# Performance work log

Hardware: AMD Instinct MI355X
Metric: run time of the kernel (lower is better)

Reference implementation:

```python
import jax, jax.numpy as jnp
import numpy as np

KH = KW = 9
BN_EPS = 1e-5


def conv3x3(x, w):
    # x: [B,Cin,H,W], w: [Cout,Cin,3,3], stride 1, padding 1
    return jax.lax.conv_general_dilated(
        x, w, window_strides=(1, 1), padding=((1, 1), (1, 1)),
        dimension_numbers=("NCHW", "OIHW", "NCHW"))


def cbr(x, w, bn):
    # bn: [4, C] rows = (gamma, beta, running_mean, running_var); inference-mode BN
    g, b, m, v = bn[0], bn[1], bn[2], bn[3]
    x = conv3x3(x, w)
    x = (x - m[:, None, None]) * (g[:, None, None] / jnp.sqrt(v[:, None, None] + BN_EPS)) + b[:, None, None]
    return jax.nn.relu(x)


def weighting(x, atten):
    # x: [B,C,H,W], atten: [B,H,W,KH*KW]
    # out[b,c,h,w] = sum_k atten[b,h,w,k] * x[b,c, h+dh(k), w+dw(k)]  (zero-padded window)
    B, C, H, W = x.shape
    patches = jax.lax.conv_general_dilated_patches(
        x, filter_shape=(KH, KW), window_strides=(1, 1),
        padding=((KH // 2, KH // 2), (KW // 2, KW // 2)))  # [B, C*KH*KW, H, W], channel-major
    patches = patches.reshape(B, C, KH * KW, H, W)
    return jnp.einsum("bckhw,bhwk->bchw", patches, atten)


def _make_params(key, fc_dim=1024):
    d4, d16 = fc_dim // 4, fc_dim // 16
    ks = jax.random.split(key, 16)
    def conv_w(k, co, ci):
        return jax.random.normal(k, (co, ci, 3, 3), jnp.float32) * (1.0 / np.sqrt(ci * 9))
    def bn(k, c):
        g = 1.0 + 0.1 * jax.random.normal(k, (c,), jnp.float32)
        return jnp.stack([g, jnp.zeros((c,)), jnp.zeros((c,)), jnp.ones((c,))])
    p = {}
    p["w1"], p["bn1"] = conv_w(ks[0], d4, fc_dim), bn(ks[1], d4)
    p["w2"], p["bn2"] = conv_w(ks[2], d16, d4), bn(ks[3], d16)
    p["w3"], p["bn3"] = conv_w(ks[4], d4, d16), bn(ks[5], d4)
    p["w4"], p["bn4"] = conv_w(ks[6], d4, fc_dim), bn(ks[7], d4)
    p["w5"], p["bn5"] = conv_w(ks[8], d4, d4), bn(ks[9], d4)
    p["fw1"] = jax.random.normal(ks[10], (10, d4), jnp.float32) * (1.0 / np.sqrt(d4))
    p["fb1"] = jnp.zeros((10,), jnp.float32)
    p["fw2"] = jax.random.normal(ks[11], (1, 10), jnp.float32) * (1.0 / np.sqrt(10))
    p["fb2"] = jnp.zeros((1,), jnp.float32)
    return p


def setup_inputs() -> dict:
    key = jax.random.key(0)
    k1, k2, k3, kp = jax.random.split(key, 4)
    B, fc_dim, H, W = 4, 1024, 64, 64
    inp = {
        "low_key": jax.random.normal(k1, (B, fc_dim, H, W), jnp.float32),
        "low_nonkey": jax.random.normal(k2, (B, fc_dim, H, W), jnp.float32),
        "local_atten": jax.random.uniform(k3, (B, H, W, KH * KW), jnp.float32),
    }
    inp.update(_make_params(kp, fc_dim))
    return inp


def reference(low_key, low_nonkey, local_atten,
              w1, bn1, w2, bn2, w3, bn3, w4, bn4, w5, bn5,
              fw1, fb1, fw2, fb2):
    x = cbr(low_key, w1, bn1)        # [B, 256, H, W]
    x = cbr(x, w2, bn2)              # [B, 64, H, W]
    x = weighting(x, local_atten)    # 9x9 local-attention weighted gather
    x = cbr(x, w3, bn3)              # [B, 256, H, W]
    y = cbr(low_nonkey, w4, bn4)     # [B, 256, H, W]
    out = cbr(x - y, w5, bn5)        # [B, 256, H, W]
    out = out.mean(axis=(2, 3))      # adaptive avg pool to 1x1 -> [B, 256]
    out = out @ fw1.T + fb1          # [B, 10]
    out = out @ fw2.T + fb2          # [B, 1]
    return out
```

## Files before the change

### kernel.cpp

```cpp
#include <hip/hip_runtime.h>
#include <math.h>

typedef _Float16 f16;
typedef f16 f16x8 __attribute__((ext_vector_type(8)));
typedef float f32x4 __attribute__((ext_vector_type(4)));

#define NB 4

__global__ void __launch_bounds__(256)
wtrans_kernel(const float* __restrict__ w, f16* __restrict__ wt, int Co, int Cin) {
  int idx = blockIdx.x * 256 + threadIdx.x;
  int total = Co * Cin * 9;
  if (idx >= total) return;
  int k = idx % 9, t2 = idx / 9;
  int ci = t2 % Cin, co = t2 / Cin;
  wt[((size_t)k * Co + co) * Cin + ci] = (f16)w[idx];
}

__global__ void __launch_bounds__(256)
nchw2nhwc(const float* __restrict__ in, f16* __restrict__ out) {
  __shared__ f16 s[64][66];
  const int t = threadIdx.x;
  const int bh = blockIdx.x, c0 = blockIdx.y * 64;
  const int b = bh >> 6, h = bh & 63;
  const int w = t & 63, cr = t >> 6;
  #pragma unroll
  for (int i = 0; i < 16; ++i) {
    int c = c0 + cr * 16 + i;
    s[cr * 16 + i][w] = (f16)in[(((size_t)b * 1024 + c) * 64 + h) * 64 + w];
  }
  __syncthreads();
  #pragma unroll
  for (int i = 0; i < 2; ++i) {
    int task = t + 256 * i;
    int oct = task & 7, w2 = task >> 3;
    f16x8 v;
    #pragma unroll
    for (int j = 0; j < 8; ++j) v[j] = s[oct * 8 + j][w2];
    *(f16x8*)(out + (((size_t)b * 64 + h) * 64 + w2) * 1024 + c0 + oct * 8) = v;
  }
}

__global__ void __launch_bounds__(256)
conv_mfma(const f16* __restrict__ in, const f16* __restrict__ in2,
          const f16* __restrict__ wt, const float* __restrict__ bn,
          f16* __restrict__ out, float* __restrict__ partial,
          int Cin, int Co) {
  __shared__ __align__(16) f16 xs[4][66][40];
  __shared__ __align__(16) f16 ws[9][64][32];
  __shared__ float s_red[4][64];

  const int t = threadIdx.x;
  const int tile = blockIdx.x;
  const int b = tile >> 5;
  const int h0 = (tile & 31) * 2;
  const int co_blk = blockIdx.y * 64;
  const int wid = t >> 6, lane = t & 63;
  const int row_w = wid >> 1, wcol = (wid & 1) * 32;
  const int l15 = lane & 15, lg = lane >> 4;
  const int koff = lg * 8;

  f32x4 acc[4][2];
  #pragma unroll
  for (int m = 0; m < 4; ++m)
    #pragma unroll
    for (int n = 0; n < 2; ++n)
      #pragma unroll
      for (int r = 0; r < 4; ++r) acc[m][n][r] = 0.f;

  const f16* inb = in + (size_t)b * Cin * 4096;
  const f16* inb2 = in2 ? in2 + (size_t)b * Cin * 4096 : nullptr;

  const int octS = t & 3, wS = (t >> 2) & 63;
  const int NC = Cin >> 5;
  f16x8 ireg[4], wreg[9];

  auto load_stage = [&](int ci0) {
    #pragma unroll
    for (int r = 0; r < 4; ++r) {
      int gh = h0 - 1 + r;
      f16x8 v = {};
      if ((unsigned)gh < 64u) {
        size_t off = ((size_t)gh * 64 + wS) * Cin + ci0 + octS * 8;
        v = *(const f16x8*)(inb + off);
        if (inb2) { f16x8 v2 = *(const f16x8*)(inb2 + off); v = v - v2; }
      }
      ireg[r] = v;
    }
    #pragma unroll
    for (int i = 0; i < 9; ++i) {
      int s = t + 256 * i;
      int oct = s & 3, co = (s >> 2) & 63, k = s >> 8;
      wreg[i] = *(const f16x8*)(wt + ((size_t)k * Co + co_blk + co) * Cin + ci0 + oct * 8);
    }
  };
  auto write_stage = [&]() {
    #pragma unroll
    for (int r = 0; r < 4; ++r)
      *(f16x8*)&xs[r][wS + 1][octS * 8] = ireg[r];
    #pragma unroll
    for (int i = 0; i < 9; ++i) {
      int s = t + 256 * i;
      int oct = s & 3, co = (s >> 2) & 63, k = s >> 8;
      *(f16x8*)&ws[k][co][oct * 8] = wreg[i];
    }
  };

  if (t < 32) {
    int r = t >> 3, side = (t >> 2) & 1, oc = t & 3;
    f16x8 z = {};
    *(f16x8*)&xs[r][side * 65][oc * 8] = z;
  }
  load_stage(0);
  write_stage();
  __syncthreads();

  for (int c = 0; c < NC; ++c) {
    if (c + 1 < NC) load_stage((c + 1) << 5);
    #pragma unroll
    for (int tap = 0; tap < 9; ++tap) {
      const int dh = tap / 3 - 1, dw = tap % 3 - 1;
      f16x8 af[4];
      #pragma unroll
      for (int m = 0; m < 4; ++m)
        af[m] = *(const f16x8*)&ws[tap][m * 16 + l15][koff];
      #pragma unroll
      for (int n = 0; n < 2; ++n) {
        const f16x8 bf = *(const f16x8*)&xs[row_w + dh + 1][wcol + n * 16 + l15 + 1 + dw][koff];
        #pragma unroll
        for (int m = 0; m < 4; ++m)
          acc[m][n] = __builtin_amdgcn_mfma_f32_16x16x32_f16(af[m], bf, acc[m][n], 0, 0, 0);
      }
    }
    __syncthreads();
    if (c + 1 < NC) write_stage();
    __syncthreads();
  }

  if (out) {
    f16* str = (f16*)xs;
    #pragma unroll
    for (int m = 0; m < 4; ++m)
      #pragma unroll
      for (int reg = 0; reg < 4; ++reg) {
        const int cwb = m * 16 + lg * 4 + reg;
        const int co = co_blk + cwb;
        float scale = bn[co] / sqrtf(bn[3 * Co + co] + 1e-5f);
        float shift = bn[Co + co] - bn[2 * Co + co] * scale;
        #pragma unroll
        for (int n = 0; n < 2; ++n) {
          float val = fmaxf(fmaf(acc[m][n][reg], scale, shift), 0.f);
          int px = row_w * 64 + wcol + n * 16 + l15;
          str[px * 72 + cwb] = (f16)val;
        }
      }
    __syncthreads();
    #pragma unroll
    for (int i = 0; i < 4; ++i) {
      int task = t + 256 * i;
      int oct = task & 7;
      int rest = task >> 3;
      int w = rest & 63, row = rest >> 6;
      f16x8 v = *(const f16x8*)&str[(row * 64 + w) * 72 + oct * 8];
      *(f16x8*)(out + (((size_t)(b * 64 + h0 + row) * 64) + w) * Co + co_blk + oct * 8) = v;
    }
  } else {
    #pragma unroll
    for (int m = 0; m < 4; ++m)
      #pragma unroll
      for (int reg = 0; reg < 4; ++reg) {
        const int cwb = m * 16 + lg * 4 + reg;
        const int co = co_blk + cwb;
        float scale = bn[co] / sqrtf(bn[3 * Co + co] + 1e-5f);
        float shift = bn[Co + co] - bn[2 * Co + co] * scale;
        float s = fmaxf(fmaf(acc[m][0][reg], scale, shift), 0.f)
                + fmaxf(fmaf(acc[m][1][reg], scale, shift), 0.f);
        s += __shfl_xor(s, 1, 64);
        s += __shfl_xor(s, 2, 64);
        s += __shfl_xor(s, 4, 64);
        s += __shfl_xor(s, 8, 64);
        if (l15 == 0) s_red[wid][cwb] = s;
      }
    __syncthreads();
    if (t < 64) {
      float v = s_red[0][t] + s_red[1][t] + s_red[2][t] + s_red[3][t];
      partial[((size_t)(b * 256) + co_blk + t) * 32 + (tile & 31)] = v;
    }
  }
}

__global__ void __launch_bounds__(256)
weighting_nhwc(const f16* __restrict__ x, const float* __restrict__ atten,
               f16* __restrict__ out) {
  __shared__ float s_a[64 * 81];
  const int h = blockIdx.x, b = blockIdx.y;
  const int t = threadIdx.x;
  for (int idx = t; idx < 64 * 81; idx += 256)
    s_a[idx] = atten[(size_t)((b * 64 + h) * 64) * 81 + idx];
  __syncthreads();

  const int w = t & 63, cg = t >> 6;
  float acc[16];
  #pragma unroll
  for (int j = 0; j < 16; ++j) acc[j] = 0.f;

  for (int dh = -4; dh <= 4; ++dh) {
    int hh = h + dh;
    if ((unsigned)hh >= 64u) continue;
    #pragma unroll
    for (int dw = -4; dw <= 4; ++dw) {
      int ww = w + dw;
      if ((unsigned)ww >= 64u) continue;
      float a = s_a[w * 81 + (dh + 4) * 9 + (dw + 4)];
      const f16* xp = x + (((size_t)b * 64 + hh) * 64 + ww) * 64 + cg * 16;
      f16x8 v0 = *(const f16x8*)xp;
      f16x8 v1 = *(const f16x8*)(xp + 8);
      #pragma unroll
      for (int j = 0; j < 8; ++j) {
        acc[j]     = fmaf(a, (float)v0[j], acc[j]);
        acc[8 + j] = fmaf(a, (float)v1[j], acc[8 + j]);
      }
    }
  }
  f16x8 o0, o1;
  #pragma unroll
  for (int j = 0; j < 8; ++j) { o0[j] = (f16)acc[j]; o1[j] = (f16)acc[8 + j]; }
  f16* op = out + (((size_t)b * 64 + h) * 64 + w) * 64 + cg * 16;
  *(f16x8*)op = o0;
  *(f16x8*)(op + 8) = o1;
}

__global__ void __launch_bounds__(256)
fc_kernel(const float* __restrict__ partial, const float* __restrict__ fw1,
          const float* __restrict__ fb1, const float* __restrict__ fw2,
          const float* __restrict__ fb2, float* __restrict__ outp) {
  const int t = threadIdx.x;
  const int b = t >> 6, lane = t & 63;
  float pooled[4];
  #pragma unroll
  for (int k = 0; k < 4; ++k) {
    int c = lane + 64 * k;
    float s = 0.f;
    #pragma unroll
    for (int p = 0; p < 32; ++p) s += partial[(size_t)(b * 256 + c) * 32 + p];
    pooled[k] = s * (1.f / 4096.f);
  }
  float o = 0.f;
  for (int i = 0; i < 10; ++i) {
    float d = 0.f;
    #pragma unroll
    for (int k = 0; k < 4; ++k) d += pooled[k] * fw1[i * 256 + lane + 64 * k];
    #pragma unroll
    for (int off = 32; off > 0; off >>= 1) d += __shfl_down(d, off, 64);
    o += (d + fb1[i]) * fw2[i];
  }
  if (lane == 0) outp[b] = o + fb2[0];
}

extern "C" void kernel_launch(void* const* d_in, const int* in_sizes, int n_in,
                              void* d_out, int out_size, void* d_ws, size_t ws_size,
                              hipStream_t stream) {
  const float* low_key    = (const float*)d_in[0];
  const float* low_nonkey = (const float*)d_in[1];
  const float* atten      = (const float*)d_in[2];
  const float* w1 = (const float*)d_in[3];  const float* bn1 = (const float*)d_in[4];
  const float* w2 = (const float*)d_in[5];  const float* bn2 = (const float*)d_in[6];
  const float* w3 = (const float*)d_in[7];  const float* bn3 = (const float*)d_in[8];
  const float* w4 = (const float*)d_in[9];  const float* bn4 = (const float*)d_in[10];
  const float* w5 = (const float*)d_in[11]; const float* bn5 = (const float*)d_in[12];
  const float* fw1 = (const float*)d_in[13]; const float* fb1 = (const float*)d_in[14];
  const float* fw2 = (const float*)d_in[15]; const float* fb2 = (const float*)d_in[16];

  f16* T   = (f16*)d_ws;
  f16* X1  = T + 16777216;
  f16* X2  = X1 + 4194304;
  f16* X3  = X2 + 1048576;
  f16* Y   = X3 + 1048576;
  f16* wt1 = Y + 4194304;
  f16* wt2 = wt1 + 2359296;
  f16* wt3 = wt2 + 147456;
  f16* wt4 = wt3 + 147456;
  f16* wt5 = wt4 + 2359296;
  float* P = (float*)(wt5 + 589824);

  dim3 blk(256);
  wtrans_kernel<<<(256 * 1024 * 9 + 255) / 256, blk, 0, stream>>>(w1, wt1, 256, 1024);
  wtrans_kernel<<<(64 * 256 * 9 + 255) / 256, blk, 0, stream>>>(w2, wt2, 64, 256);
  wtrans_kernel<<<(256 * 64 * 9 + 255) / 256, blk, 0, stream>>>(w3, wt3, 256, 64);
  wtrans_kernel<<<(256 * 1024 * 9 + 255) / 256, blk, 0, stream>>>(w4, wt4, 256, 1024);
  wtrans_kernel<<<(256 * 256 * 9 + 255) / 256, blk, 0, stream>>>(w5, wt5, 256, 256);

  nchw2nhwc<<<dim3(256, 16), blk, 0, stream>>>(low_key, T);
  conv_mfma<<<dim3(128, 4), blk, 0, stream>>>(T, nullptr, wt1, bn1, X1, nullptr, 1024, 256);
  conv_mfma<<<dim3(128, 1), blk, 0, stream>>>(X1, nullptr, wt2, bn2, X2, nullptr, 256, 64);
  weighting_nhwc<<<dim3(64, NB), blk, 0, stream>>>(X2, atten, X3);
  conv_mfma<<<dim3(128, 4), blk, 0, stream>>>(X3, nullptr, wt3, bn3, X1, nullptr, 64, 256);
  nchw2nhwc<<<dim3(256, 16), blk, 0, stream>>>(low_nonkey, T);
  conv_mfma<<<dim3(128, 4), blk, 0, stream>>>(T, nullptr, wt4, bn4, Y, nullptr, 1024, 256);
  conv_mfma<<<dim3(128, 4), blk, 0, stream>>>(X1, Y, wt5, bn5, nullptr, P, 256, 256);
  fc_kernel<<<1, 256, 0, stream>>>(P, fw1, fb1, fw2, fb2, (float*)d_out);
}
```

Baseline: 344.7 us.

## Enlarge conv tile to four rows per block and write output directly

Each conv block now computes four output rows instead of two, with each wave owning a full 64-wide row and 16 accumulators. The weight tile staged in LDS is reused across twice as many pixels, and halo overhead per output drops. The epilogue writes f16x4 straight to global memory instead of staging through shared memory. The weight transpose kernel is also reindexed so its writes are coalesced. In exchange the grid is halved (256 blocks for the big convs, 64 for conv2), which may underfill the 256 CUs, and register pressure rises.

```diff
diff --git a/kernel.cpp b/kernel.cpp
--- a/kernel.cpp
+++ b/kernel.cpp
@@ -2,6 +2,7 @@
 #include <math.h>
 
 typedef _Float16 f16;
+typedef f16 f16x4 __attribute__((ext_vector_type(4)));
 typedef f16 f16x8 __attribute__((ext_vector_type(8)));
 typedef float f32x4 __attribute__((ext_vector_type(4)));
 
@@ -12,9 +13,9 @@
   int idx = blockIdx.x * 256 + threadIdx.x;
   int total = Co * Cin * 9;
   if (idx >= total) return;
-  int k = idx % 9, t2 = idx / 9;
-  int ci = t2 % Cin, co = t2 / Cin;
-  wt[((size_t)k * Co + co) * Cin + ci] = (f16)w[idx];
+  int ci = idx % Cin, t2 = idx / Cin;
+  int co = t2 % Co, k = t2 / Co;
+  wt[idx] = (f16)w[((size_t)co * Cin + ci) * 9 + k];
 }
 
 __global__ void __launch_bounds__(256)
@@ -46,38 +47,37 @@
           const f16* __restrict__ wt, const float* __restrict__ bn,
           f16* __restrict__ out, float* __restrict__ partial,
           int Cin, int Co) {
-  __shared__ __align__(16) f16 xs[4][66][40];
+  __shared__ __align__(16) f16 xs[6][66][40];
   __shared__ __align__(16) f16 ws[9][64][32];
   __shared__ float s_red[4][64];
 
   const int t = threadIdx.x;
   const int tile = blockIdx.x;
-  const int b = tile >> 5;
-  const int h0 = (tile & 31) * 2;
+  const int b = tile >> 4;
+  const int h0 = (tile & 15) * 4;
   const int co_blk = blockIdx.y * 64;
   const int wid = t >> 6, lane = t & 63;
-  const int row_w = wid >> 1, wcol = (wid & 1) * 32;
   const int l15 = lane & 15, lg = lane >> 4;
   const int koff = lg * 8;
 
-  f32x4 acc[4][2];
+  f32x4 acc[4][4];
   #pragma unroll
   for (int m = 0; m < 4; ++m)
     #pragma unroll
-    for (int n = 0; n < 2; ++n)
+    for (int n = 0; n < 4; ++n)
       #pragma unroll
       for (int r = 0; r < 4; ++r) acc[m][n][r] = 0.f;
 
   const f16* inb = in + (size_t)b * Cin * 4096;
   const f16* inb2 = in2 ? in2 + (size_t)b * Cin * 4096 : nullptr;
 
-  const int octS = t & 3, wS = (t >> 2) & 63;
+  const int wS = t >> 2, octS = t & 3;
   const int NC = Cin >> 5;
-  f16x8 ireg[4], wreg[9];
+  f16x8 ireg[6], wreg[9];
 
   auto load_stage = [&](int ci0) {
     #pragma unroll
-    for (int r = 0; r < 4; ++r) {
+    for (int r = 0; r < 6; ++r) {
       int gh = h0 - 1 + r;
       f16x8 v = {};
       if ((unsigned)gh < 64u) {
@@ -96,7 +96,7 @@
   };
   auto write_stage = [&]() {
     #pragma unroll
-    for (int r = 0; r < 4; ++r)
+    for (int r = 0; r < 6; ++r)
       *(f16x8*)&xs[r][wS + 1][octS * 8] = ireg[r];
     #pragma unroll
     for (int i = 0; i < 9; ++i) {
@@ -106,7 +106,7 @@
     }
   };
 
-  if (t < 32) {
+  if (t < 48) {
     int r = t >> 3, side = (t >> 2) & 1, oc = t & 3;
     f16x8 z = {};
     *(f16x8*)&xs[r][side * 65][oc * 8] = z;
@@ -125,8 +125,8 @@
       for (int m = 0; m < 4; ++m)
         af[m] = *(const f16x8*)&ws[tap][m * 16 + l15][koff];
       #pragma unroll
-      for (int n = 0; n < 2; ++n) {
-        const f16x8 bf = *(const f16x8*)&xs[row_w + dh + 1][wcol + n * 16 + l15 + 1 + dw][koff];
+      for (int n = 0; n < 4; ++n) {
+        const f16x8 bf = *(const f16x8*)&xs[wid + dh + 1][n * 16 + l15 + 1 + dw][koff];
         #pragma unroll
         for (int m = 0; m < 4; ++m)
           acc[m][n] = __builtin_amdgcn_mfma_f32_16x16x32_f16(af[m], bf, acc[m][n], 0, 0, 0);
@@ -138,53 +138,47 @@
   }
 
   if (out) {
-    f16* str = (f16*)xs;
+    #pragma unroll
+    for (int m = 0; m < 4; ++m) {
+      float sc[4], sh[4];
+      #pragma unroll
+      for (int reg = 0; reg < 4; ++reg) {
+        int co = co_blk + m * 16 + lg * 4 + reg;
+        sc[reg] = bn[co] / sqrtf(bn[3 * Co + co] + 1e-5f);
+        sh[reg] = bn[Co + co] - bn[2 * Co + co] * sc[reg];
+      }
+      #pragma unroll
+      for (int n = 0; n < 4; ++n) {
+        f16x4 v;
+        #pragma unroll
+        for (int reg = 0; reg < 4; ++reg)
+          v[reg] = (f16)fmaxf(fmaf(acc[m][n][reg], sc[reg], sh[reg]), 0.f);
+        *(f16x4*)(out + ((size_t)(b * 64 + h0 + wid) * 64 + n * 16 + l15) * Co
+                      + co_blk + m * 16 + lg * 4) = v;
+      }
+    }
+  } else {
     #pragma unroll
     for (int m = 0; m < 4; ++m)
       #pragma unroll
       for (int reg = 0; reg < 4; ++reg) {
-        const int cwb = m * 16 + lg * 4 + reg;
-        const int co = co_blk + cwb;
-        float scale = bn[co] / sqrtf(bn[3 * Co + co] + 1e-5f);
-        float shift = bn[Co + co] - bn[2 * Co + co] * scale;
+        int co = co_blk + m * 16 + lg * 4 + reg;
+        float sc = bn[co] / sqrtf(bn[3 * Co + co] + 1e-5f);
+        float sh = bn[Co + co] - bn[2 * Co + co] * sc;
+        float s = 0.f;
         #pragma unroll
-        for (int n = 0; n < 2; ++n) {
-          float val = fmaxf(fmaf(acc[m][n][reg], scale, shift), 0.f);
-          int px = row_w * 64 + wcol + n * 16 + l15;
-          str[px * 72 + cwb] = (f16)val;
-        }
-      }
-    __syncthreads();
-    #pragma unroll
-    for (int i = 0; i < 4; ++i) {
-      int task = t + 256 * i;
-      int oct = task & 7;
-      int rest = task >> 3;
-      int w = rest & 63, row = rest >> 6;
-      f16x8 v = *(const f16x8*)&str[(row * 64 + w) * 72 + oct * 8];
-      *(f16x8*)(out + (((size_t)(b * 64 + h0 + row) * 64) + w) * Co + co_blk + oct * 8) = v;
-    }
-  } else {
-    #pragma unroll
-    for (int m = 0; m < 4; ++m)
-      #pragma unroll
-      for (int reg = 0; reg < 4; ++reg) {
-        const int cwb = m * 16 + lg * 4 + reg;
-        const int co = co_blk + cwb;
-        float scale = bn[co] / sqrtf(bn[3 * Co + co] + 1e-5f);
-        float shift = bn[Co + co] - bn[2 * Co + co] * scale;
-        float s = fmaxf(fmaf(acc[m][0][reg], scale, shift), 0.f)
-                + fmaxf(fmaf(acc[m][1][reg], scale, shift), 0.f);
+        for (int n = 0; n < 4; ++n)
+          s += fmaxf(fmaf(acc[m][n][reg], sc, sh), 0.f);
         s += __shfl_xor(s, 1, 64);
         s += __shfl_xor(s, 2, 64);
         s += __shfl_xor(s, 4, 64);
         s += __shfl_xor(s, 8, 64);
-        if (l15 == 0) s_red[wid][cwb] = s;
+        if (l15 == 0) s_red[wid][m * 16 + lg * 4 + reg] = s;
       }
     __syncthreads();
     if (t < 64) {
       float v = s_red[0][t] + s_red[1][t] + s_red[2][t] + s_red[3][t];
-      partial[((size_t)(b * 256) + co_blk + t) * 32 + (tile & 31)] = v;
+      partial[((size_t)b * Co + co_blk + t) * 16 + (tile & 15)] = v;
     }
   }
 }
@@ -242,7 +236,7 @@
     int c = lane + 64 * k;
     float s = 0.f;
     #pragma unroll
-    for (int p = 0; p < 32; ++p) s += partial[(size_t)(b * 256 + c) * 32 + p];
+    for (int p = 0; p < 16; ++p) s += partial[(size_t)(b * 256 + c) * 16 + p];
     pooled[k] = s * (1.f / 4096.f);
   }
   float o = 0.f;
@@ -291,12 +285,12 @@
   wtrans_kernel<<<(256 * 256 * 9 + 255) / 256, blk, 0, stream>>>(w5, wt5, 256, 256);
 
   nchw2nhwc<<<dim3(256, 16), blk, 0, stream>>>(low_key, T);
-  conv_mfma<<<dim3(128, 4), blk, 0, stream>>>(T, nullptr, wt1, bn1, X1, nullptr, 1024, 256);
-  conv_mfma<<<dim3(128, 1), blk, 0, stream>>>(X1, nullptr, wt2, bn2, X2, nullptr, 256, 64);
+  conv_mfma<<<dim3(64, 4), blk, 0, stream>>>(T, nullptr, wt1, bn1, X1, nullptr, 1024, 256);
+  conv_mfma<<<dim3(64, 1), blk, 0, stream>>>(X1, nullptr, wt2, bn2, X2, nullptr, 256, 64);
   weighting_nhwc<<<dim3(64, NB), blk, 0, stream>>>(X2, atten, X3);
-  conv_mfma<<<dim3(128, 4), blk, 0, stream>>>(X3, nullptr, wt3, bn3, X1, nullptr, 64, 256);
+  conv_mfma<<<dim3(64, 4), blk, 0, stream>>>(X3, nullptr, wt3, bn3, X1, nullptr, 64, 256);
   nchw2nhwc<<<dim3(256, 16), blk, 0, stream>>>(low_nonkey, T);
-  conv_mfma<<<dim3(128, 4), blk, 0, stream>>>(T, nullptr, wt4, bn4, Y, nullptr, 1024, 256);
-  conv_mfma<<<dim3(128, 4), blk, 0, stream>>>(X1, Y, wt5, bn5, nullptr, P, 256, 256);
+  conv_mfma<<<dim3(64, 4), blk, 0, stream>>>(T, nullptr, wt4, bn4, Y, nullptr, 1024, 256);
+  conv_mfma<<<dim3(64, 4), blk, 0, stream>>>(X1, Y, wt5, bn5, nullptr, P, 256, 256);
   fc_kernel<<<1, 256, 0, stream>>>(P, fw1, fb1, fw2, fb2, (float*)d_out);
 }
```

Result: faster. 326.7 us (-5.2%).
